# Kernel optimization log

Measured on AMD Instinct MI355X. Metric: run time of the kernel, lower is better.

## Reference

```python
import jax, jax.numpy as jnp
import numpy as np

HEAD_SIZE = 256
HEAD_SIZE_R = HEAD_SIZE // 4   # 64, RoPE slice
HEAD_SIZE_C = HEAD_SIZE - HEAD_SIZE_R  # 192
N_EMBD = 256


def rope(x, start_pos=0):
    # x: [B, T, d_r] with interleaved (even, odd) pairs
    B, T, d = x.shape
    half = d // 2
    theta = 1.0 / (10000.0 ** (jnp.arange(half, dtype=x.dtype) / half))  # [half]
    idx = jnp.arange(start_pos, start_pos + T, dtype=x.dtype)[:, None] * theta[None, :]  # [T, half]
    sin, cos = jnp.sin(idx), jnp.cos(idx)
    xs = x.reshape(B, T, half, 2)
    x1, x2 = xs[..., 0], xs[..., 1]
    rot = jnp.stack([x1 * cos - x2 * sin, x1 * sin + x2 * cos], axis=-1)
    return rot.reshape(B, T, d)


def setup_inputs() -> dict:
    key = jax.random.key(0)
    ks = jax.random.split(key, 8)
    B, T = 32, 2048
    s = 0.05
    return {
        "x": jax.random.normal(ks[0], (B, T, N_EMBD), dtype=jnp.float32),
        "Wq_comp": jax.random.normal(ks[1], (N_EMBD, N_EMBD), dtype=jnp.float32) * s,
        "Wkv_comp": jax.random.normal(ks[2], (N_EMBD, N_EMBD), dtype=jnp.float32) * s,
        "Wqc": jax.random.normal(ks[3], (N_EMBD, HEAD_SIZE_C), dtype=jnp.float32) * s,
        "Wqr": jax.random.normal(ks[4], (N_EMBD, HEAD_SIZE_R), dtype=jnp.float32) * s,
        "Wkc": jax.random.normal(ks[5], (N_EMBD, HEAD_SIZE_C), dtype=jnp.float32) * s,
        "Wkr": jax.random.normal(ks[6], (N_EMBD, HEAD_SIZE_R), dtype=jnp.float32) * s,
        "Wv": jax.random.normal(ks[7], (N_EMBD, HEAD_SIZE), dtype=jnp.float32) * s,
    }


def reference(x, Wq_comp, Wkv_comp, Wqc, Wqr, Wkc, Wkr, Wv):
    # Low-rank compression
    c_q = x @ Wq_comp      # [B,T,C]
    c_kv = x @ Wkv_comp    # [B,T,C]
    # Q: content + rotary slice
    q_c = c_q @ Wqc                      # [B,T,192]
    q_r = rope(c_q @ Wqr, start_pos=0)   # [B,T,64]
    q = jnp.concatenate([q_c, q_r], axis=-1)  # [B,T,256]
    # K: content + rotary slice
    k_c = c_kv @ Wkc
    k_r = rope(c_kv @ Wkr, start_pos=0)
    k = jnp.concatenate([k_c, k_r], axis=-1)  # [B,T,256]
    v = c_kv @ Wv                              # [B,T,256]
    # Causal attention (dropout is identity in eval)
    scale = 1.0 / jnp.sqrt(jnp.asarray(HEAD_SIZE, dtype=x.dtype))
    wei = jnp.einsum('bqd,bkd->bqk', q, k) * scale  # [B,T,T]
    T_q = q.shape[1]
    mask = jnp.tril(jnp.ones((T_q, T_q), dtype=bool))
    wei = jnp.where(mask, wei, jnp.asarray(-jnp.inf, dtype=wei.dtype))
    wei = jax.nn.softmax(wei, axis=-1)
    out = jnp.einsum('bqk,bkd->bqd', wei, v)  # [B,T,256]
    return out, (k, v)
```

## Files before the change

kernel.cpp:

```cpp
#include <hip/hip_runtime.h>

typedef float  f32x4  __attribute__((ext_vector_type(4)));
typedef __bf16 bf16x8 __attribute__((ext_vector_type(8)));
typedef unsigned short u16x8 __attribute__((ext_vector_type(8)));
typedef unsigned short u16x4 __attribute__((ext_vector_type(4)));

#define DEV static __device__ __forceinline__

DEV unsigned short f2b(float f) {
  unsigned int u = __float_as_uint(f);
  u += 0x7fffu + ((u >> 16) & 1u);
  return (unsigned short)(u >> 16);
}
DEV float b2f(unsigned short h) { return __uint_as_float(((unsigned int)h) << 16); }

DEV f32x4 mfma16(bf16x8 a, bf16x8 b, f32x4 c) {
  return __builtin_amdgcn_mfma_f32_16x16x32_bf16(a, b, c, 0, 0, 0);
}

__global__ __launch_bounds__(256) void k_prep(
    const float* __restrict__ Wq_comp, const float* __restrict__ Wkv_comp,
    const float* __restrict__ Wqc, const float* __restrict__ Wqr,
    const float* __restrict__ Wkc, const float* __restrict__ Wkr,
    const float* __restrict__ Wv,
    unsigned short* __restrict__ W1t, unsigned short* __restrict__ Wqt,
    unsigned short* __restrict__ Wkvt, float* __restrict__ ct, float* __restrict__ st) {
  int tid = blockIdx.x * 256 + threadIdx.x;
  if (tid < 131072) {
    int n = tid >> 8, k = tid & 255;
    float v = (n < 256) ? Wq_comp[k * 256 + n] : Wkv_comp[k * 256 + (n - 256)];
    W1t[tid] = f2b(v);
  } else if (tid < 196608) {
    int t2 = tid - 131072; int n = t2 >> 8, k = t2 & 255;
    float v = (n < 192) ? Wqc[k * 192 + n] : Wqr[k * 64 + (n - 192)];
    Wqt[t2] = f2b(v);
  } else if (tid < 327680) {
    int t2 = tid - 196608; int n = t2 >> 8, k = t2 & 255;
    float v = (n < 192) ? Wkc[k * 192 + n]
             : (n < 256) ? Wkr[k * 64 + (n - 192)] : Wv[k * 256 + (n - 256)];
    Wkvt[t2] = f2b(v);
  } else if (tid < 393216) {
    int t2 = tid - 327680; int t = t2 >> 5, i = t2 & 31;
    float theta = powf(10000.0f, -(float)i / 32.0f);
    float ang = (float)t * theta;
    ct[t2] = cosf(ang); st[t2] = sinf(ang);
  }
}

__global__ __launch_bounds__(256) void k_gemm1(const float* __restrict__ X,
    const unsigned short* __restrict__ Bt, unsigned short* __restrict__ C) {
  __shared__ __align__(16) unsigned short Ash[128 * 72];
  __shared__ __align__(16) unsigned short Bsh[128 * 72];
  const int nt = blockIdx.x, mt = blockIdx.y;
  const int tid = threadIdx.x;
  const int l = tid & 63, wv = tid >> 6, li = l & 15, g = l >> 4;
  const int wm = wv >> 1, wn = wv & 1;
  const f32x4 zf = {0.f, 0.f, 0.f, 0.f};
  f32x4 acc[4][4];
#pragma unroll
  for (int i = 0; i < 4; ++i)
#pragma unroll
    for (int j = 0; j < 4; ++j) acc[i][j] = zf;
  for (int kb = 0; kb < 256; kb += 64) {
    __syncthreads();
#pragma unroll
    for (int it = 0; it < 8; ++it) {
      int idx = it * 256 + tid;
      int row = idx >> 4, c4 = (idx & 15) << 2;
      f32x4 v = *reinterpret_cast<const f32x4*>(X + (size_t)(mt * 128 + row) * 256 + kb + c4);
      u16x4 u = { f2b(v.x), f2b(v.y), f2b(v.z), f2b(v.w) };
      *reinterpret_cast<u16x4*>(&Ash[row * 72 + c4]) = u;
    }
#pragma unroll
    for (int it = 0; it < 4; ++it) {
      int idx = it * 256 + tid;
      int row = idx >> 3, c8 = (idx & 7) << 3;
      *reinterpret_cast<u16x8*>(&Bsh[row * 72 + c8]) =
        *reinterpret_cast<const u16x8*>(Bt + (size_t)(nt * 128 + row) * 256 + kb + c8);
    }
    __syncthreads();
#pragma unroll
    for (int kc = 0; kc < 2; ++kc) {
      bf16x8 a[4], b[4];
#pragma unroll
      for (int mf = 0; mf < 4; ++mf)
        a[mf] = *reinterpret_cast<const bf16x8*>(&Ash[(wm * 64 + mf * 16 + li) * 72 + kc * 32 + g * 8]);
#pragma unroll
      for (int nf = 0; nf < 4; ++nf)
        b[nf] = *reinterpret_cast<const bf16x8*>(&Bsh[(wn * 64 + nf * 16 + li) * 72 + kc * 32 + g * 8]);
#pragma unroll
      for (int mf = 0; mf < 4; ++mf)
#pragma unroll
        for (int nf = 0; nf < 4; ++nf)
          acc[mf][nf] = mfma16(a[mf], b[nf], acc[mf][nf]);
    }
  }
#pragma unroll
  for (int mf = 0; mf < 4; ++mf)
#pragma unroll
    for (int nf = 0; nf < 4; ++nf)
#pragma unroll
      for (int r = 0; r < 4; ++r) {
        int row = mt * 128 + wm * 64 + mf * 16 + g * 4 + r;
        int col = nt * 128 + wn * 64 + nf * 16 + li;
        C[(size_t)row * 512 + col] = f2b(acc[mf][nf][r]);
      }
}

__global__ __launch_bounds__(256) void k_gemm2(const unsigned short* __restrict__ C12,
    const unsigned short* __restrict__ Wqt, const unsigned short* __restrict__ Wkvt,
    unsigned short* __restrict__ q_ws, unsigned short* __restrict__ k_ws,
    float* __restrict__ kout, float* __restrict__ vout,
    const float* __restrict__ ct, const float* __restrict__ st) {
  __shared__ __align__(16) unsigned short Ash[128 * 72];
  __shared__ __align__(16) unsigned short Bsh[128 * 72];
  const int nt = blockIdx.x, mt = blockIdx.y;
  const int tid = threadIdx.x;
  const int l = tid & 63, wv = tid >> 6, li = l & 15, g = l >> 4;
  const int wm = wv >> 1, wn = wv & 1;
  const int acol = (nt < 2) ? 0 : 256;
  const unsigned short* Wt = (nt < 2) ? Wqt : Wkvt;
  const int wrow = (nt < 2) ? nt * 128 : (nt - 2) * 128;
  const f32x4 zf = {0.f, 0.f, 0.f, 0.f};
  f32x4 acc[4][4];
#pragma unroll
  for (int i = 0; i < 4; ++i)
#pragma unroll
    for (int j = 0; j < 4; ++j) acc[i][j] = zf;
  for (int kb = 0; kb < 256; kb += 64) {
    __syncthreads();
#pragma unroll
    for (int it = 0; it < 4; ++it) {
      int idx = it * 256 + tid;
      int row = idx >> 3, c8 = (idx & 7) << 3;
      *reinterpret_cast<u16x8*>(&Ash[row * 72 + c8]) =
        *reinterpret_cast<const u16x8*>(C12 + (size_t)(mt * 128 + row) * 512 + acol + kb + c8);
    }
#pragma unroll
    for (int it = 0; it < 4; ++it) {
      int idx = it * 256 + tid;
      int row = idx >> 3, c8 = (idx & 7) << 3;
      *reinterpret_cast<u16x8*>(&Bsh[row * 72 + c8]) =
        *reinterpret_cast<const u16x8*>(Wt + (size_t)(wrow + row) * 256 + kb + c8);
    }
    __syncthreads();
#pragma unroll
    for (int kc = 0; kc < 2; ++kc) {
      bf16x8 a[4], b[4];
#pragma unroll
      for (int mf = 0; mf < 4; ++mf)
        a[mf] = *reinterpret_cast<const bf16x8*>(&Ash[(wm * 64 + mf * 16 + li) * 72 + kc * 32 + g * 8]);
#pragma unroll
      for (int nf = 0; nf < 4; ++nf)
        b[nf] = *reinterpret_cast<const bf16x8*>(&Bsh[(wn * 64 + nf * 16 + li) * 72 + kc * 32 + g * 8]);
#pragma unroll
      for (int mf = 0; mf < 4; ++mf)
#pragma unroll
        for (int nf = 0; nf < 4; ++nf)
          acc[mf][nf] = mfma16(a[mf], b[nf], acc[mf][nf]);
    }
  }
  if ((nt == 1 || nt == 3) && wn == 1) {
#pragma unroll
    for (int mf = 0; mf < 4; ++mf)
#pragma unroll
      for (int nf = 0; nf < 4; ++nf)
#pragma unroll
        for (int r = 0; r < 4; ++r) {
          float v = acc[mf][nf][r];
          float other = __shfl_xor(v, 1);
          int t = (mt * 128 + wm * 64 + mf * 16 + g * 4 + r) & 2047;
          int i = nf * 8 + (li >> 1);
          float c = ct[t * 32 + i], s = st[t * 32 + i];
          acc[mf][nf][r] = (li & 1) ? (other * s + v * c) : (v * c - other * s);
        }
  }
#pragma unroll
  for (int mf = 0; mf < 4; ++mf)
#pragma unroll
    for (int nf = 0; nf < 4; ++nf) {
      int col = nt * 128 + wn * 64 + nf * 16 + li;
#pragma unroll
      for (int r = 0; r < 4; ++r) {
        int row = mt * 128 + wm * 64 + mf * 16 + g * 4 + r;
        float val = acc[mf][nf][r];
        if (col < 256) {
          q_ws[(size_t)row * 256 + col] = f2b(val);
        } else if (col < 512) {
          k_ws[(size_t)row * 256 + (col - 256)] = f2b(val);
          kout[(size_t)row * 256 + (col - 256)] = val;
        } else {
          vout[(size_t)row * 256 + (col - 512)] = val;
        }
      }
    }
}

__global__ __launch_bounds__(256) void k_vtrans(const float* __restrict__ vout,
                                                unsigned short* __restrict__ vt) {
  __shared__ float tile[32][33];
  const int dt = blockIdx.x, tt = blockIdx.y, b = blockIdx.z;
  const int tid = threadIdx.x;
#pragma unroll
  for (int it = 0; it < 4; ++it) {
    int idx = it * 256 + tid;
    int tr = idx >> 5, dc = idx & 31;
    tile[tr][dc] = vout[((size_t)b * 2048 + tt * 32 + tr) * 256 + dt * 32 + dc];
  }
  __syncthreads();
#pragma unroll
  for (int it = 0; it < 4; ++it) {
    int idx = it * 256 + tid;
    int dr = idx >> 5, tc = idx & 31;
    vt[((size_t)b * 256 + dt * 32 + dr) * 2048 + tt * 32 + tc] = f2b(tile[tc][dr]);
  }
}

__global__ __launch_bounds__(512, 2) void k_attn(
    const unsigned short* __restrict__ q_ws, const unsigned short* __restrict__ k_ws,
    const unsigned short* __restrict__ vt_ws, float* __restrict__ out) {
  __shared__ __align__(16) unsigned short Ksh[64 * 256];
  __shared__ __align__(16) unsigned short Vsh[256 * 64];
  __shared__ __align__(16) unsigned short Psh[8][1024];
  const int b = blockIdx.x;
  const int p = blockIdx.y;
  const int tid = threadIdx.x;
  const int l = tid & 63, wv = tid >> 6, li = l & 15, g = l >> 4;
  const f32x4 zf = {0.f, 0.f, 0.f, 0.f};

  u16x8 ones_u = {0x3F80, 0x3F80, 0x3F80, 0x3F80, 0x3F80, 0x3F80, 0x3F80, 0x3F80};
  bf16x8 ones = *reinterpret_cast<bf16x8*>(&ones_u);

  const int s_kr = tid >> 5, s_kc = tid & 31;
  const int s_kpc = s_kc ^ (s_kr & 7);
  const int s_vd = tid >> 3, s_vc = tid & 7;
  const int s_vpc = s_vc ^ (s_vd & 7);

  const unsigned short* kbase = k_ws + (size_t)b * 2048 * 256;
  const unsigned short* vbase = vt_ws + (size_t)b * 256 * 2048;

  u16x8 kreg[4], vreg[4];

  for (int seg = 0; seg < 2; ++seg) {
    const int qt = seg ? (15 - p) : p;
    const int wq0 = qt * 128 + wv * 16;
    bf16x8 qf[8];
    const unsigned short* qp = q_ws + ((size_t)b * 2048 + wq0 + li) * 256;
#pragma unroll
    for (int kc = 0; kc < 8; ++kc)
      qf[kc] = *reinterpret_cast<const bf16x8*>(qp + kc * 32 + g * 8);

    f32x4 o[16];
#pragma unroll
    for (int i = 0; i < 16; ++i) o[i] = zf;
    f32x4 ol = zf;

    const int nj = 2 * qt + 2;
#pragma unroll
    for (int it = 0; it < 4; ++it)
      kreg[it] = *reinterpret_cast<const u16x8*>(kbase + (size_t)(s_kr + it * 16) * 256 + s_kc * 8);
#pragma unroll
    for (int it = 0; it < 4; ++it)
      vreg[it] = *reinterpret_cast<const u16x8*>(vbase + (size_t)(s_vd + it * 64) * 2048 + s_vc * 8);

    for (int j = 0; j < nj; ++j) {
      __syncthreads();
#pragma unroll
      for (int it = 0; it < 4; ++it)
        *reinterpret_cast<u16x8*>(&Ksh[(s_kr + it * 16) * 256 + s_kpc * 8]) = kreg[it];
#pragma unroll
      for (int it = 0; it < 4; ++it)
        *reinterpret_cast<u16x8*>(&Vsh[(s_vd + it * 64) * 64 + s_vpc * 8]) = vreg[it];
      __syncthreads();
      if (j + 1 < nj) {
        const unsigned short* kb2 = kbase + (size_t)(j + 1) * 64 * 256;
        const unsigned short* vb2 = vbase + (size_t)(j + 1) * 64;
#pragma unroll
        for (int it = 0; it < 4; ++it)
          kreg[it] = *reinterpret_cast<const u16x8*>(kb2 + (size_t)(s_kr + it * 16) * 256 + s_kc * 8);
#pragma unroll
        for (int it = 0; it < 4; ++it)
          vreg[it] = *reinterpret_cast<const u16x8*>(vb2 + (size_t)(s_vd + it * 64) * 2048 + s_vc * 8);
      }
      if (j * 64 > qt * 128 + wv * 16 + 15) continue;

      f32x4 s[4];
#pragma unroll
      for (int nf = 0; nf < 4; ++nf) s[nf] = zf;
#pragma unroll
      for (int kc = 0; kc < 8; ++kc) {
        int pc = (kc * 4 + g) ^ (li & 7);
#pragma unroll
        for (int nf = 0; nf < 4; ++nf) {
          bf16x8 bk = *reinterpret_cast<const bf16x8*>(&Ksh[(nf * 16 + li) * 256 + pc * 8]);
          s[nf] = mfma16(qf[kc], bk, s[nf]);
        }
      }
#pragma unroll
      for (int r = 0; r < 4; ++r) {
        const int q = g * 4 + r;
        const int qg = wv * 16 + q;
#pragma unroll
        for (int nf = 0; nf < 4; ++nf) {
          int kg = j * 64 + nf * 16 + li - qt * 128;
          float pv = __expf(__builtin_fmaf(s[nf][r], 0.0625f, -8.0f));
          if (kg > qg) pv = 0.f;
          int kk = nf * 16 + li;
          int pcp = (kk >> 3) ^ (q & 7);
          Psh[wv][q * 64 + pcp * 8 + (kk & 7)] = f2b(pv);
        }
      }
#pragma unroll
      for (int kc2 = 0; kc2 < 2; ++kc2) {
        int pcp = (kc2 * 4 + g) ^ (li & 7);
        bf16x8 pa = *reinterpret_cast<const bf16x8*>(&Psh[wv][li * 64 + pcp * 8]);
        ol = mfma16(pa, ones, ol);
#pragma unroll
        for (int nfd = 0; nfd < 16; ++nfd) {
          bf16x8 bv = *reinterpret_cast<const bf16x8*>(&Vsh[(nfd * 16 + li) * 64 + pcp * 8]);
          o[nfd] = mfma16(pa, bv, o[nfd]);
        }
      }
    }

#pragma unroll
    for (int r = 0; r < 4; ++r) {
      float inv = 1.0f / ol[r];
      int qrow = wq0 + g * 4 + r;
      float* op = out + ((size_t)b * 2048 + qrow) * 256;
#pragma unroll
      for (int nfd = 0; nfd < 16; ++nfd)
        op[nfd * 16 + li] = o[nfd][r] * inv;
    }
  }
}

extern "C" void kernel_launch(void* const* d_in, const int* in_sizes, int n_in,
                              void* d_out, int out_size, void* d_ws, size_t ws_size,
                              hipStream_t stream) {
  const float* x        = (const float*)d_in[0];
  const float* Wq_comp  = (const float*)d_in[1];
  const float* Wkv_comp = (const float*)d_in[2];
  const float* Wqc      = (const float*)d_in[3];
  const float* Wqr      = (const float*)d_in[4];
  const float* Wkc      = (const float*)d_in[5];
  const float* Wkr      = (const float*)d_in[6];
  const float* Wv       = (const float*)d_in[7];

  float* out  = (float*)d_out;
  float* kout = out + 16777216;
  float* vout = out + 33554432;

  if (ws_size < 135397376u) return;

  char* ws = (char*)d_ws;
  unsigned short* C12  = (unsigned short*)(ws);
  unsigned short* vt   = (unsigned short*)(ws);
  unsigned short* q_ws = (unsigned short*)(ws + 67108864);
  unsigned short* k_ws = (unsigned short*)(ws + 100663296);
  unsigned short* W1t  = (unsigned short*)(ws + 134217728);
  unsigned short* Wqt  = W1t + 131072;
  unsigned short* Wkvt = Wqt + 65536;
  float* ct = (float*)(Wkvt + 131072);
  float* st = ct + 65536;

  k_prep<<<1536, 256, 0, stream>>>(Wq_comp, Wkv_comp, Wqc, Wqr, Wkc, Wkr, Wv,
                                   W1t, Wqt, Wkvt, ct, st);
  k_gemm1<<<dim3(4, 512), 256, 0, stream>>>(x, W1t, C12);
  k_gemm2<<<dim3(6, 512), 256, 0, stream>>>(C12, Wqt, Wkvt, q_ws, k_ws, kout, vout, ct, st);
  k_vtrans<<<dim3(8, 64, 32), 256, 0, stream>>>(vout, vt);
  k_attn<<<dim3(32, 8), 512, 0, stream>>>(q_ws, k_ws, vt, out);
}
```

Baseline: 276.2 us.

## Double-buffer attention K/V via direct global-to-LDS loads and widen GEMM tiles

The attention kernel now uses 4 waves, each handling 32 query rows, so every K/V fragment read from LDS feeds two MFMAs. K and V tiles are double-buffered and loaded directly into LDS with global_load_lds, replacing the register-staged copies, so one barrier per tile overlaps the next tile's load with compute. Both projection GEMMs move to 512-thread blocks with 128x256 tiles, halving the grid and reusing each A tile across twice as many output columns. The trade-off is more LDS per block and fewer waves to hide latency in attention, plus new swizzled P and LDS addressing that must stay correct.

```diff
diff --git a/kernel.cpp b/kernel.cpp
--- a/kernel.cpp
+++ b/kernel.cpp
@@ -16,6 +16,12 @@
 
 DEV f32x4 mfma16(bf16x8 a, bf16x8 b, f32x4 c) {
   return __builtin_amdgcn_mfma_f32_16x16x32_bf16(a, b, c, 0, 0, 0);
+}
+
+typedef __attribute__((address_space(1))) const unsigned int* gas_t;
+typedef __attribute__((address_space(3))) unsigned int* las_t;
+DEV void gl16(const void* g, void* l) {
+  __builtin_amdgcn_global_load_lds((gas_t)g, (las_t)l, 16, 0, 0);
 }
 
 __global__ __launch_bounds__(256) void k_prep(
@@ -47,14 +53,14 @@
   }
 }
 
-__global__ __launch_bounds__(256) void k_gemm1(const float* __restrict__ X,
+__global__ __launch_bounds__(512, 2) void k_gemm1(const float* __restrict__ X,
     const unsigned short* __restrict__ Bt, unsigned short* __restrict__ C) {
   __shared__ __align__(16) unsigned short Ash[128 * 72];
-  __shared__ __align__(16) unsigned short Bsh[128 * 72];
-  const int nt = blockIdx.x, mt = blockIdx.y;
+  __shared__ __align__(16) unsigned short Bsh[256 * 72];
+  const int nt2 = blockIdx.x, mt = blockIdx.y;
   const int tid = threadIdx.x;
   const int l = tid & 63, wv = tid >> 6, li = l & 15, g = l >> 4;
-  const int wm = wv >> 1, wn = wv & 1;
+  const int wm = wv >> 2, wn = wv & 3;
   const f32x4 zf = {0.f, 0.f, 0.f, 0.f};
   f32x4 acc[4][4];
 #pragma unroll
@@ -64,8 +70,8 @@
   for (int kb = 0; kb < 256; kb += 64) {
     __syncthreads();
 #pragma unroll
-    for (int it = 0; it < 8; ++it) {
-      int idx = it * 256 + tid;
+    for (int it = 0; it < 4; ++it) {
+      int idx = it * 512 + tid;
       int row = idx >> 4, c4 = (idx & 15) << 2;
       f32x4 v = *reinterpret_cast<const f32x4*>(X + (size_t)(mt * 128 + row) * 256 + kb + c4);
       u16x4 u = { f2b(v.x), f2b(v.y), f2b(v.z), f2b(v.w) };
@@ -73,10 +79,10 @@
     }
 #pragma unroll
     for (int it = 0; it < 4; ++it) {
-      int idx = it * 256 + tid;
+      int idx = it * 512 + tid;
       int row = idx >> 3, c8 = (idx & 7) << 3;
       *reinterpret_cast<u16x8*>(&Bsh[row * 72 + c8]) =
-        *reinterpret_cast<const u16x8*>(Bt + (size_t)(nt * 128 + row) * 256 + kb + c8);
+        *reinterpret_cast<const u16x8*>(Bt + (size_t)(nt2 * 256 + row) * 256 + kb + c8);
     }
     __syncthreads();
 #pragma unroll
@@ -102,25 +108,25 @@
 #pragma unroll
       for (int r = 0; r < 4; ++r) {
         int row = mt * 128 + wm * 64 + mf * 16 + g * 4 + r;
-        int col = nt * 128 + wn * 64 + nf * 16 + li;
+        int col = nt2 * 256 + wn * 64 + nf * 16 + li;
         C[(size_t)row * 512 + col] = f2b(acc[mf][nf][r]);
       }
 }
 
-__global__ __launch_bounds__(256) void k_gemm2(const unsigned short* __restrict__ C12,
+__global__ __launch_bounds__(512, 2) void k_gemm2(const unsigned short* __restrict__ C12,
     const unsigned short* __restrict__ Wqt, const unsigned short* __restrict__ Wkvt,
     unsigned short* __restrict__ q_ws, unsigned short* __restrict__ k_ws,
     float* __restrict__ kout, float* __restrict__ vout,
     const float* __restrict__ ct, const float* __restrict__ st) {
   __shared__ __align__(16) unsigned short Ash[128 * 72];
-  __shared__ __align__(16) unsigned short Bsh[128 * 72];
-  const int nt = blockIdx.x, mt = blockIdx.y;
+  __shared__ __align__(16) unsigned short Bsh[256 * 72];
+  const int sel = blockIdx.x, mt = blockIdx.y;
   const int tid = threadIdx.x;
   const int l = tid & 63, wv = tid >> 6, li = l & 15, g = l >> 4;
-  const int wm = wv >> 1, wn = wv & 1;
-  const int acol = (nt < 2) ? 0 : 256;
-  const unsigned short* Wt = (nt < 2) ? Wqt : Wkvt;
-  const int wrow = (nt < 2) ? nt * 128 : (nt - 2) * 128;
+  const int wm = wv >> 2, wn = wv & 3;
+  const int acol = (sel == 0) ? 0 : 256;
+  const unsigned short* Wt = (sel == 0) ? Wqt : Wkvt;
+  const int wrow = (sel == 2) ? 256 : 0;
   const f32x4 zf = {0.f, 0.f, 0.f, 0.f};
   f32x4 acc[4][4];
 #pragma unroll
@@ -130,15 +136,15 @@
   for (int kb = 0; kb < 256; kb += 64) {
     __syncthreads();
 #pragma unroll
-    for (int it = 0; it < 4; ++it) {
-      int idx = it * 256 + tid;
+    for (int it = 0; it < 2; ++it) {
+      int idx = it * 512 + tid;
       int row = idx >> 3, c8 = (idx & 7) << 3;
       *reinterpret_cast<u16x8*>(&Ash[row * 72 + c8]) =
         *reinterpret_cast<const u16x8*>(C12 + (size_t)(mt * 128 + row) * 512 + acol + kb + c8);
     }
 #pragma unroll
     for (int it = 0; it < 4; ++it) {
-      int idx = it * 256 + tid;
+      int idx = it * 512 + tid;
       int row = idx >> 3, c8 = (idx & 7) << 3;
       *reinterpret_cast<u16x8*>(&Bsh[row * 72 + c8]) =
         *reinterpret_cast<const u16x8*>(Wt + (size_t)(wrow + row) * 256 + kb + c8);
@@ -160,7 +166,7 @@
           acc[mf][nf] = mfma16(a[mf], b[nf], acc[mf][nf]);
     }
   }
-  if ((nt == 1 || nt == 3) && wn == 1) {
+  if (sel < 2 && wn == 3) {
 #pragma unroll
     for (int mf = 0; mf < 4; ++mf)
 #pragma unroll
@@ -179,18 +185,18 @@
   for (int mf = 0; mf < 4; ++mf)
 #pragma unroll
     for (int nf = 0; nf < 4; ++nf) {
-      int col = nt * 128 + wn * 64 + nf * 16 + li;
+      int cl = wn * 64 + nf * 16 + li;
 #pragma unroll
       for (int r = 0; r < 4; ++r) {
         int row = mt * 128 + wm * 64 + mf * 16 + g * 4 + r;
         float val = acc[mf][nf][r];
-        if (col < 256) {
-          q_ws[(size_t)row * 256 + col] = f2b(val);
-        } else if (col < 512) {
-          k_ws[(size_t)row * 256 + (col - 256)] = f2b(val);
-          kout[(size_t)row * 256 + (col - 256)] = val;
+        if (sel == 0) {
+          q_ws[(size_t)row * 256 + cl] = f2b(val);
+        } else if (sel == 1) {
+          k_ws[(size_t)row * 256 + cl] = f2b(val);
+          kout[(size_t)row * 256 + cl] = val;
         } else {
-          vout[(size_t)row * 256 + (col - 512)] = val;
+          vout[(size_t)row * 256 + cl] = val;
         }
       }
     }
@@ -216,14 +222,13 @@
   }
 }
 
-__global__ __launch_bounds__(512, 2) void k_attn(
+__global__ __launch_bounds__(256, 1) void k_attn(
     const unsigned short* __restrict__ q_ws, const unsigned short* __restrict__ k_ws,
     const unsigned short* __restrict__ vt_ws, float* __restrict__ out) {
-  __shared__ __align__(16) unsigned short Ksh[64 * 256];
-  __shared__ __align__(16) unsigned short Vsh[256 * 64];
-  __shared__ __align__(16) unsigned short Psh[8][1024];
-  const int b = blockIdx.x;
-  const int p = blockIdx.y;
+  __shared__ __align__(16) unsigned short Kb[2][64 * 256];
+  __shared__ __align__(16) unsigned short Vb[2][256 * 64];
+  __shared__ __align__(16) unsigned short Psh[4][1024];
+  const int b = blockIdx.x, p = blockIdx.y;
   const int tid = threadIdx.x;
   const int l = tid & 63, wv = tid >> 6, li = l & 15, g = l >> 4;
   const f32x4 zf = {0.f, 0.f, 0.f, 0.f};
@@ -231,108 +236,119 @@
   u16x8 ones_u = {0x3F80, 0x3F80, 0x3F80, 0x3F80, 0x3F80, 0x3F80, 0x3F80, 0x3F80};
   bf16x8 ones = *reinterpret_cast<bf16x8*>(&ones_u);
 
-  const int s_kr = tid >> 5, s_kc = tid & 31;
-  const int s_kpc = s_kc ^ (s_kr & 7);
-  const int s_vd = tid >> 3, s_vc = tid & 7;
-  const int s_vpc = s_vc ^ (s_vd & 7);
-
   const unsigned short* kbase = k_ws + (size_t)b * 2048 * 256;
   const unsigned short* vbase = vt_ws + (size_t)b * 256 * 2048;
 
-  u16x8 kreg[4], vreg[4];
+#define STAGE(t, Kdst, Vdst)                                                          \
+  {                                                                                   \
+    const unsigned short* ks_ = kbase + (size_t)(t) * 64 * 256;                       \
+    const unsigned short* vs_ = vbase + (size_t)(t) * 64;                             \
+    _Pragma("unroll")                                                                 \
+    for (int rnd = 0; rnd < 8; ++rnd) {                                               \
+      int chunk = rnd * 256 + wv * 64 + l;                                            \
+      int row = chunk >> 5, pc = chunk & 31;                                          \
+      gl16(ks_ + (size_t)row * 256 + ((pc ^ (row & 7)) << 3),                         \
+           (Kdst) + (size_t)(rnd * 256 + wv * 64) * 8);                               \
+    }                                                                                 \
+    _Pragma("unroll")                                                                 \
+    for (int rnd = 0; rnd < 8; ++rnd) {                                               \
+      int chunk = rnd * 256 + wv * 64 + l;                                            \
+      int d = chunk >> 3, pc = chunk & 7;                                             \
+      gl16(vs_ + (size_t)d * 2048 + ((pc ^ (d & 7)) << 3),                            \
+           (Vdst) + (size_t)(rnd * 256 + wv * 64) * 8);                               \
+    }                                                                                 \
+  }
 
   for (int seg = 0; seg < 2; ++seg) {
     const int qt = seg ? (15 - p) : p;
-    const int wq0 = qt * 128 + wv * 16;
-    bf16x8 qf[8];
-    const unsigned short* qp = q_ws + ((size_t)b * 2048 + wq0 + li) * 256;
-#pragma unroll
-    for (int kc = 0; kc < 8; ++kc)
-      qf[kc] = *reinterpret_cast<const bf16x8*>(qp + kc * 32 + g * 8);
-
-    f32x4 o[16];
-#pragma unroll
-    for (int i = 0; i < 16; ++i) o[i] = zf;
-    f32x4 ol = zf;
+    const int wq0 = qt * 128 + wv * 32;
+    bf16x8 qf[2][8];
+#pragma unroll
+    for (int mf = 0; mf < 2; ++mf) {
+      const unsigned short* qp = q_ws + ((size_t)b * 2048 + wq0 + mf * 16 + li) * 256;
+#pragma unroll
+      for (int kc = 0; kc < 8; ++kc)
+        qf[mf][kc] = *reinterpret_cast<const bf16x8*>(qp + kc * 32 + g * 8);
+    }
+
+    f32x4 o[2][16];
+#pragma unroll
+    for (int i = 0; i < 2; ++i)
+#pragma unroll
+      for (int j2 = 0; j2 < 16; ++j2) o[i][j2] = zf;
+    f32x4 ol[2] = {zf, zf};
 
     const int nj = 2 * qt + 2;
-#pragma unroll
-    for (int it = 0; it < 4; ++it)
-      kreg[it] = *reinterpret_cast<const u16x8*>(kbase + (size_t)(s_kr + it * 16) * 256 + s_kc * 8);
-#pragma unroll
-    for (int it = 0; it < 4; ++it)
-      vreg[it] = *reinterpret_cast<const u16x8*>(vbase + (size_t)(s_vd + it * 64) * 2048 + s_vc * 8);
+    STAGE(0, Kb[0], Vb[0]);
+    __syncthreads();
 
     for (int j = 0; j < nj; ++j) {
-      __syncthreads();
-#pragma unroll
-      for (int it = 0; it < 4; ++it)
-        *reinterpret_cast<u16x8*>(&Ksh[(s_kr + it * 16) * 256 + s_kpc * 8]) = kreg[it];
-#pragma unroll
-      for (int it = 0; it < 4; ++it)
-        *reinterpret_cast<u16x8*>(&Vsh[(s_vd + it * 64) * 64 + s_vpc * 8]) = vreg[it];
-      __syncthreads();
-      if (j + 1 < nj) {
-        const unsigned short* kb2 = kbase + (size_t)(j + 1) * 64 * 256;
-        const unsigned short* vb2 = vbase + (size_t)(j + 1) * 64;
-#pragma unroll
-        for (int it = 0; it < 4; ++it)
-          kreg[it] = *reinterpret_cast<const u16x8*>(kb2 + (size_t)(s_kr + it * 16) * 256 + s_kc * 8);
-#pragma unroll
-        for (int it = 0; it < 4; ++it)
-          vreg[it] = *reinterpret_cast<const u16x8*>(vb2 + (size_t)(s_vd + it * 64) * 2048 + s_vc * 8);
-      }
-      if (j * 64 > qt * 128 + wv * 16 + 15) continue;
-
-      f32x4 s[4];
-#pragma unroll
-      for (int nf = 0; nf < 4; ++nf) s[nf] = zf;
-#pragma unroll
-      for (int kc = 0; kc < 8; ++kc) {
-        int pc = (kc * 4 + g) ^ (li & 7);
-#pragma unroll
-        for (int nf = 0; nf < 4; ++nf) {
-          bf16x8 bk = *reinterpret_cast<const bf16x8*>(&Ksh[(nf * 16 + li) * 256 + pc * 8]);
-          s[nf] = mfma16(qf[kc], bk, s[nf]);
+      const int c = j & 1;
+      if (j + 1 < nj) STAGE(j + 1, Kb[c ^ 1], Vb[c ^ 1]);
+
+      if (j * 64 - qt * 128 <= wv * 32 + 31) {
+        f32x4 s[2][4];
+#pragma unroll
+        for (int mf = 0; mf < 2; ++mf)
+#pragma unroll
+          for (int nf = 0; nf < 4; ++nf) s[mf][nf] = zf;
+#pragma unroll
+        for (int kc = 0; kc < 8; ++kc) {
+          int pc = (kc * 4 + g) ^ (li & 7);
+#pragma unroll
+          for (int nf = 0; nf < 4; ++nf) {
+            bf16x8 bk = *reinterpret_cast<const bf16x8*>(&Kb[c][(nf * 16 + li) * 256 + pc * 8]);
+            s[0][nf] = mfma16(qf[0][kc], bk, s[0][nf]);
+            s[1][nf] = mfma16(qf[1][kc], bk, s[1][nf]);
+          }
+        }
+#pragma unroll
+        for (int h = 0; h < 2; ++h) {
+#pragma unroll
+          for (int mf = 0; mf < 2; ++mf)
+#pragma unroll
+            for (int r = 0; r < 4; ++r) {
+              const int q = mf * 16 + g * 4 + r;
+              const int qg = wv * 32 + q;
+#pragma unroll
+              for (int nf2 = 0; nf2 < 2; ++nf2) {
+                const int nf = h * 2 + nf2;
+                float pv = __expf(__builtin_fmaf(s[mf][nf][r], 0.0625f, -8.0f));
+                int kg = j * 64 + nf * 16 + li - qt * 128;
+                if (kg > qg) pv = 0.f;
+                int kkl = nf2 * 16 + li;
+                Psh[wv][q * 32 + (((kkl >> 3) ^ (q & 3)) << 3) + (kkl & 7)] = f2b(pv);
+              }
+            }
+          bf16x8 pa0 = *reinterpret_cast<const bf16x8*>(&Psh[wv][li * 32 + ((g ^ (li & 3)) << 3)]);
+          bf16x8 pa1 = *reinterpret_cast<const bf16x8*>(&Psh[wv][(16 + li) * 32 + ((g ^ (li & 3)) << 3)]);
+          ol[0] = mfma16(pa0, ones, ol[0]);
+          ol[1] = mfma16(pa1, ones, ol[1]);
+          int pcv = (h * 4 + g) ^ (li & 7);
+#pragma unroll
+          for (int nfd = 0; nfd < 16; ++nfd) {
+            bf16x8 bv = *reinterpret_cast<const bf16x8*>(&Vb[c][(nfd * 16 + li) * 64 + pcv * 8]);
+            o[0][nfd] = mfma16(pa0, bv, o[0][nfd]);
+            o[1][nfd] = mfma16(pa1, bv, o[1][nfd]);
+          }
         }
       }
+      __syncthreads();
+    }
+
+#pragma unroll
+    for (int mf = 0; mf < 2; ++mf)
 #pragma unroll
       for (int r = 0; r < 4; ++r) {
-        const int q = g * 4 + r;
-        const int qg = wv * 16 + q;
-#pragma unroll
-        for (int nf = 0; nf < 4; ++nf) {
-          int kg = j * 64 + nf * 16 + li - qt * 128;
-          float pv = __expf(__builtin_fmaf(s[nf][r], 0.0625f, -8.0f));
-          if (kg > qg) pv = 0.f;
-          int kk = nf * 16 + li;
-          int pcp = (kk >> 3) ^ (q & 7);
-          Psh[wv][q * 64 + pcp * 8 + (kk & 7)] = f2b(pv);
-        }
+        float inv = 1.0f / ol[mf][r];
+        int qrow = wq0 + mf * 16 + g * 4 + r;
+        float* op = out + ((size_t)b * 2048 + qrow) * 256;
+#pragma unroll
+        for (int nfd = 0; nfd < 16; ++nfd)
+          op[nfd * 16 + li] = o[mf][nfd][r] * inv;
       }
-#pragma unroll
-      for (int kc2 = 0; kc2 < 2; ++kc2) {
-        int pcp = (kc2 * 4 + g) ^ (li & 7);
-        bf16x8 pa = *reinterpret_cast<const bf16x8*>(&Psh[wv][li * 64 + pcp * 8]);
-        ol = mfma16(pa, ones, ol);
-#pragma unroll
-        for (int nfd = 0; nfd < 16; ++nfd) {
-          bf16x8 bv = *reinterpret_cast<const bf16x8*>(&Vsh[(nfd * 16 + li) * 64 + pcp * 8]);
-          o[nfd] = mfma16(pa, bv, o[nfd]);
-        }
-      }
-    }
-
-#pragma unroll
-    for (int r = 0; r < 4; ++r) {
-      float inv = 1.0f / ol[r];
-      int qrow = wq0 + g * 4 + r;
-      float* op = out + ((size_t)b * 2048 + qrow) * 256;
-#pragma unroll
-      for (int nfd = 0; nfd < 16; ++nfd)
-        op[nfd * 16 + li] = o[nfd][r] * inv;
-    }
-  }
+  }
+#undef STAGE
 }
 
 extern "C" void kernel_launch(void* const* d_in, const int* in_sizes, int n_in,
@@ -366,8 +382,8 @@
 
   k_prep<<<1536, 256, 0, stream>>>(Wq_comp, Wkv_comp, Wqc, Wqr, Wkc, Wkr, Wv,
                                    W1t, Wqt, Wkvt, ct, st);
-  k_gemm1<<<dim3(4, 512), 256, 0, stream>>>(x, W1t, C12);
-  k_gemm2<<<dim3(6, 512), 256, 0, stream>>>(C12, Wqt, Wkvt, q_ws, k_ws, kout, vout, ct, st);
+  k_gemm1<<<dim3(2, 512), 512, 0, stream>>>(x, W1t, C12);
+  k_gemm2<<<dim3(3, 512), 512, 0, stream>>>(C12, Wqt, Wkvt, q_ws, k_ws, kout, vout, ct, st);
   k_vtrans<<<dim3(8, 64, 32), 256, 0, stream>>>(vout, vt);
-  k_attn<<<dim3(32, 8), 512, 0, stream>>>(q_ws, k_ws, vt, out);
-}
+  k_attn<<<dim3(32, 8), 256, 0, stream>>>(q_ws, k_ws, vt, out);
+}
```

Result: slower. 322.4 us (+16.7%).
